# Performance work log

Measured on AMD Instinct MI355X. Metric: run time of the kernel, lower is better.

The kernel has to match this reference:

```python
import jax, jax.numpy as jnp
import numpy as np

N, IN_DIM, HID, OUT = 8192, 512, 256, 64
NEG_INF = -9e15


def setup_inputs() -> dict:
    key = jax.random.key(0)
    ks = jax.random.split(key, 7)
    X = jax.random.normal(ks[0], (N, IN_DIM), dtype=jnp.float32)
    A = jax.random.randint(ks[1], (N, N), 0, 2, dtype=jnp.int32)
    # fc1 (Linear): kaiming-uniform-ish init, exact dist irrelevant for correctness
    W1 = jax.random.normal(ks[2], (IN_DIM, HID), dtype=jnp.float32) / np.sqrt(IN_DIM)
    b1 = jnp.zeros((HID,), dtype=jnp.float32)
    # attention vector a: xavier_uniform(gain=1.414) on shape (2*HID, 1)
    lim = 1.414 * np.sqrt(6.0 / (2 * HID + 1))
    a = jax.random.uniform(ks[3], (2 * HID, 1), minval=-lim, maxval=lim, dtype=jnp.float32)
    Omega = jax.random.normal(ks[4], (HID, OUT), dtype=jnp.float32) * np.sqrt(2.0 / (HID + OUT))
    beta = jnp.zeros((OUT,), dtype=jnp.float32)
    return {"X": X, "A": A, "W1": W1, "b1": b1, "a": a, "Omega": Omega, "beta": beta}


def reference(X, A, W1, b1, a, Omega, beta):
    H1 = X @ W1 + b1                      # [N, HID]
    # score(i,j) = leakyrelu(a[:HID].H1_i + a[HID:].H1_j) -- computed via broadcast,
    # avoiding the O(N^2 * 2*HID) concat the torch code materializes.
    a1 = a[:HID, 0]                       # [HID]
    a2 = a[HID:, 0]                       # [HID]
    e = jax.nn.leaky_relu((H1 @ a1)[:, None] + (H1 @ a2)[None, :], negative_slope=0.2)  # [N, N]
    e = jnp.where(A > 0, e, NEG_INF)
    attention = jax.nn.softmax(e, axis=1)  # dropout_rate=0.0 -> identity
    H2 = attention @ H1                    # [N, HID]
    return jax.nn.sigmoid(H2 @ Omega + beta)  # [N, OUT]
```

## Files before the change

### kernel.cpp

```cpp
#include <hip/hip_runtime.h>
#include <hip/hip_bf16.h>


typedef float f32x4 __attribute__((ext_vector_type(4)));
typedef short s16x8 __attribute__((ext_vector_type(8)));

#define NN 8192
#define INDIM 512
#define HIDD 256
#define OUTD 64

static __device__ __forceinline__ short f2bf(float x) {
    __hip_bfloat16 h = __float2bfloat16(x);
    return __builtin_bit_cast(short, h);
}

static __device__ __forceinline__ void split_bf(float x, short& hi, short& lo) {
    short h = f2bf(x);
    unsigned int hb = ((unsigned int)(unsigned short)h) << 16;
    float hf = __builtin_bit_cast(float, hb);
    hi = h;
    lo = f2bf(x - hf);
}

__global__ void k_prepX(const float* __restrict__ X, short* __restrict__ XBhi) {
    int t = blockIdx.x * 256 + threadIdx.x;
    int r = t >> 9, k = t & 511;
    XBhi[(r >> 4) * 8192 + (k >> 3) * 128 + (r & 15) * 8 + (k & 7)] = f2bf(X[t]);
}

__global__ void k_prepW(const float* __restrict__ W1,
                        short* __restrict__ WBhi, short* __restrict__ WBlo) {
    int t = blockIdx.x * 256 + threadIdx.x;
    int k = t >> 8, n = t & 255;
    short h, l; split_bf(W1[t], h, l);
    int idx = (n >> 4) * 8192 + (k >> 3) * 128 + (n & 15) * 8 + (k & 7);
    WBhi[idx] = h;
    WBlo[idx] = l;
}

__global__ void __launch_bounds__(256, 2)
k_h1(const short* __restrict__ XBhi, const short* __restrict__ WBhi,
     const short* __restrict__ WBlo, const float* __restrict__ b1,
     const float* __restrict__ avec, unsigned short* __restrict__ H1TB,
     float* __restrict__ alw, float* __restrict__ bew, float* __restrict__ uvw) {
    __shared__ float s1p[4][16];
    __shared__ float s2p[4][16];
    const int tid = threadIdx.x;
    const int wn = tid >> 6, lane = tid & 63;
    const int q = lane >> 4, m16 = lane & 15;
    const int blk = blockIdx.x;

    f32x4 zero4 = {0.f, 0.f, 0.f, 0.f};
    f32x4 acc[4];
#pragma unroll
    for (int nt = 0; nt < 4; ++nt) acc[nt] = zero4;

    const short* xh = XBhi + blk * 8192 + q * 128 + m16 * 8;
    const short* wh = WBhi + wn * 4 * 8192 + q * 128 + m16 * 8;
    const short* wl = WBlo + wn * 4 * 8192 + q * 128 + m16 * 8;

    for (int c = 0; c < 16; ++c) {
        s16x8 ahi = *(const s16x8*)(xh + c * 512);
#pragma unroll
        for (int nt = 0; nt < 4; ++nt) {
            s16x8 bhi = *(const s16x8*)(wh + nt * 8192 + c * 512);
            s16x8 blo = *(const s16x8*)(wl + nt * 8192 + c * 512);
            acc[nt] = __builtin_amdgcn_mfma_f32_16x16x32_bf16(ahi, bhi, acc[nt], 0, 0, 0);
            acc[nt] = __builtin_amdgcn_mfma_f32_16x16x32_bf16(ahi, blo, acc[nt], 0, 0, 0);
        }
    }

    float p1[4] = {0.f, 0.f, 0.f, 0.f};
    float p2[4] = {0.f, 0.f, 0.f, 0.f};
#pragma unroll
    for (int nt = 0; nt < 4; ++nt) {
        const int col = wn * 64 + nt * 16 + m16;
        const float b1v = b1[col];
        const float a1v = avec[col];
        const float a2v = avec[HIDD + col];
        float v0 = acc[nt][0] + b1v;
        float v1 = acc[nt][1] + b1v;
        float v2 = acc[nt][2] + b1v;
        float v3 = acc[nt][3] + b1v;
        ushort4 us;
        us.x = (unsigned short)f2bf(v0);
        us.y = (unsigned short)f2bf(v1);
        us.z = (unsigned short)f2bf(v2);
        us.w = (unsigned short)f2bf(v3);
        const int idx = ((wn * 4 + nt) * 1024 + blk * 2 + (q >> 1)) * 128
                        + m16 * 8 + (q & 1) * 4;
        *(ushort4*)(H1TB + idx) = us;
        p1[0] += v0 * a1v; p1[1] += v1 * a1v; p1[2] += v2 * a1v; p1[3] += v3 * a1v;
        p2[0] += v0 * a2v; p2[1] += v1 * a2v; p2[2] += v2 * a2v; p2[3] += v3 * a2v;
    }
#pragma unroll
    for (int off = 1; off < 16; off <<= 1) {
#pragma unroll
        for (int r = 0; r < 4; ++r) {
            p1[r] += __shfl_xor(p1[r], off);
            p2[r] += __shfl_xor(p2[r], off);
        }
    }
    if (m16 == 0) {
#pragma unroll
        for (int r = 0; r < 4; ++r) {
            s1p[wn][q * 4 + r] = p1[r];
            s2p[wn][q * 4 + r] = p2[r];
        }
    }
    __syncthreads();
    if (tid < 16) {
        const int i = blk * 16 + tid;
        float s1 = s1p[0][tid] + s1p[1][tid] + s1p[2][tid] + s1p[3][tid];
        float s2 = s2p[0][tid] + s2p[1][tid] + s2p[2][tid] + s2p[3][tid];
        alw[i] = expf(s1);
        bew[i] = expf(0.2f * s1);
        uvw[2 * i]     = expf(s2);
        uvw[2 * i + 1] = expf(0.2f * s2);
    }
}

__global__ void __launch_bounds__(256, 4)
k_attn(const int* __restrict__ A, const unsigned short* __restrict__ H1TB,
       const float* __restrict__ alw, const float* __restrict__ bew,
       const float* __restrict__ uvw,
       float* __restrict__ H2acc, float* __restrict__ Zw) {
    const int tid = threadIdx.x;
    const int wn = tid >> 6, lane = tid & 63;
    const int q = lane >> 4, m16 = lane & 15;
    const int ks = blockIdx.x & 7;
    const int mb = blockIdx.x >> 3;
    const int row0 = mb * 32 + m16, row1 = row0 + 16;
    const float al0 = alw[row0], be0 = bew[row0];
    const float al1 = alw[row1], be1 = bew[row1];
    const int j0 = ks * 1024;

    const int* Ap0 = A + (size_t)row0 * NN + j0 + q * 8;
    const int* Ap1 = A + (size_t)row1 * NN + j0 + q * 8;
    const float* uvp = uvw + 2 * (j0 + q * 8);
    const unsigned short* Hp = H1TB + ((size_t)(wn * 4) * 1024 + ks * 128 + q) * 128 + m16 * 8;

    f32x4 zero4 = {0.f, 0.f, 0.f, 0.f};
    f32x4 acc[8];
#pragma unroll
    for (int i = 0; i < 8; ++i) acc[i] = zero4;
    float z0 = 0.f, z1 = 0.f;

    int4 a00 = *(const int4*)(Ap0);
    int4 a01 = *(const int4*)(Ap0 + 4);
    int4 a10 = *(const int4*)(Ap1);
    int4 a11 = *(const int4*)(Ap1 + 4);

    for (int t = 0; t < 32; ++t) {
        int4 n00, n01, n10, n11;
        if (t < 31) {
            n00 = *(const int4*)(Ap0 + 32);
            n01 = *(const int4*)(Ap0 + 36);
            n10 = *(const int4*)(Ap1 + 32);
            n11 = *(const int4*)(Ap1 + 36);
        }
        float4 uv0 = *(const float4*)(uvp);
        float4 uv1 = *(const float4*)(uvp + 4);
        float4 uv2 = *(const float4*)(uvp + 8);
        float4 uv3 = *(const float4*)(uvp + 12);

        float w0[8], w1[8];
        w0[0] = (a00.x > 0) ? fmaxf(al0 * uv0.x, be0 * uv0.y) : 0.f;
        w0[1] = (a00.y > 0) ? fmaxf(al0 * uv0.z, be0 * uv0.w) : 0.f;
        w0[2] = (a00.z > 0) ? fmaxf(al0 * uv1.x, be0 * uv1.y) : 0.f;
        w0[3] = (a00.w > 0) ? fmaxf(al0 * uv1.z, be0 * uv1.w) : 0.f;
        w0[4] = (a01.x > 0) ? fmaxf(al0 * uv2.x, be0 * uv2.y) : 0.f;
        w0[5] = (a01.y > 0) ? fmaxf(al0 * uv2.z, be0 * uv2.w) : 0.f;
        w0[6] = (a01.z > 0) ? fmaxf(al0 * uv3.x, be0 * uv3.y) : 0.f;
        w0[7] = (a01.w > 0) ? fmaxf(al0 * uv3.z, be0 * uv3.w) : 0.f;
        w1[0] = (a10.x > 0) ? fmaxf(al1 * uv0.x, be1 * uv0.y) : 0.f;
        w1[1] = (a10.y > 0) ? fmaxf(al1 * uv0.z, be1 * uv0.w) : 0.f;
        w1[2] = (a10.z > 0) ? fmaxf(al1 * uv1.x, be1 * uv1.y) : 0.f;
        w1[3] = (a10.w > 0) ? fmaxf(al1 * uv1.z, be1 * uv1.w) : 0.f;
        w1[4] = (a11.x > 0) ? fmaxf(al1 * uv2.x, be1 * uv2.y) : 0.f;
        w1[5] = (a11.y > 0) ? fmaxf(al1 * uv2.z, be1 * uv2.w) : 0.f;
        w1[6] = (a11.z > 0) ? fmaxf(al1 * uv3.x, be1 * uv3.y) : 0.f;
        w1[7] = (a11.w > 0) ? fmaxf(al1 * uv3.z, be1 * uv3.w) : 0.f;
        z0 += (w0[0] + w0[1] + w0[2] + w0[3]) + (w0[4] + w0[5] + w0[6] + w0[7]);
        z1 += (w1[0] + w1[1] + w1[2] + w1[3]) + (w1[4] + w1[5] + w1[6] + w1[7]);

        s16x8 af0, af1;
#pragma unroll
        for (int j = 0; j < 8; ++j) { af0[j] = f2bf(w0[j]); af1[j] = f2bf(w1[j]); }

#pragma unroll
        for (int nt = 0; nt < 4; ++nt) {
            s16x8 bf = *(const s16x8*)(Hp + (size_t)nt * 131072 + t * 512);
            acc[nt * 2 + 0] = __builtin_amdgcn_mfma_f32_16x16x32_bf16(af0, bf, acc[nt * 2 + 0], 0, 0, 0);
            acc[nt * 2 + 1] = __builtin_amdgcn_mfma_f32_16x16x32_bf16(af1, bf, acc[nt * 2 + 1], 0, 0, 0);
        }
        if (t < 31) { a00 = n00; a01 = n01; a10 = n10; a11 = n11; }
        Ap0 += 32; Ap1 += 32; uvp += 64;
    }

    z0 += __shfl_xor(z0, 16); z0 += __shfl_xor(z0, 32);
    z1 += __shfl_xor(z1, 16); z1 += __shfl_xor(z1, 32);
    if (wn == 0 && q == 0) {
        atomicAdd(&Zw[row0], z0);
        atomicAdd(&Zw[row1], z1);
    }

#pragma unroll
    for (int nt = 0; nt < 4; ++nt) {
        const int col = wn * 64 + nt * 16 + m16;
#pragma unroll
        for (int rg = 0; rg < 2; ++rg) {
            const int rowb = mb * 32 + rg * 16 + q * 4;
#pragma unroll
            for (int r = 0; r < 4; ++r)
                atomicAdd(&H2acc[(size_t)(rowb + r) * HIDD + col], acc[nt * 2 + rg][r]);
        }
    }
}

__global__ void __launch_bounds__(256)
k_out(const float* __restrict__ H2acc, const float* __restrict__ Zw,
      const float* __restrict__ Omega, const float* __restrict__ beta,
      float* __restrict__ out) {
    __shared__ float om[HIDD * OUTD];
    const int tid = threadIdx.x;
    for (int idx = tid; idx < HIDD * OUTD; idx += 256) om[idx] = Omega[idx];
    __syncthreads();
    const int wave = tid >> 6, o = tid & 63;
    const int i0 = blockIdx.x * 32 + wave * 8;
    float acc[8] = {0.f, 0.f, 0.f, 0.f, 0.f, 0.f, 0.f, 0.f};
    for (int c = 0; c < HIDD; c += 4) {
        const float o0 = om[(c + 0) * OUTD + o];
        const float o1 = om[(c + 1) * OUTD + o];
        const float o2 = om[(c + 2) * OUTD + o];
        const float o3 = om[(c + 3) * OUTD + o];
#pragma unroll
        for (int r = 0; r < 8; ++r) {
            float4 h = *(const float4*)(H2acc + (size_t)(i0 + r) * HIDD + c);
            acc[r] = fmaf(h.x, o0, fmaf(h.y, o1, fmaf(h.z, o2, fmaf(h.w, o3, acc[r]))));
        }
    }
    const float bv = beta[o];
#pragma unroll
    for (int r = 0; r < 8; ++r) {
        const float logit = acc[r] / Zw[i0 + r] + bv;
        out[(size_t)(i0 + r) * OUTD + o] = 1.0f / (1.0f + expf(-logit));
    }
}

extern "C" void kernel_launch(void* const* d_in, const int* in_sizes, int n_in,
                              void* d_out, int out_size, void* d_ws, size_t ws_size,
                              hipStream_t stream) {
    const float* X     = (const float*)d_in[0];
    const int*   A     = (const int*)d_in[1];
    const float* W1    = (const float*)d_in[2];
    const float* b1    = (const float*)d_in[3];
    const float* avec  = (const float*)d_in[4];
    const float* Omega = (const float*)d_in[5];
    const float* beta  = (const float*)d_in[6];
    float* out = (float*)d_out;

    char* ws = (char*)d_ws;
    unsigned short* H1TB = (unsigned short*)(ws + 0);
    short* XBhi  = (short*)(ws + 4194304);
    float* Zw    = (float*)(ws + 4194304);
    float* H2acc = (float*)(ws + 4227072);
    short* WBhi  = (short*)(ws + 12615680);
    short* WBlo  = (short*)(ws + 12877824);
    float* alw   = (float*)(ws + 13139968);
    float* bew   = (float*)(ws + 13172736);
    float* uvw   = (float*)(ws + 13205504);

    k_prepX<<<16384, 256, 0, stream>>>(X, XBhi);
    k_prepW<<<512, 256, 0, stream>>>(W1, WBhi, WBlo);
    k_h1<<<512, 256, 0, stream>>>(XBhi, WBhi, WBlo, b1, avec, H1TB, alw, bew, uvw);
    hipMemsetAsync(Zw, 0, 32768 + 8388608, stream);
    k_attn<<<2048, 256, 0, stream>>>(A, H1TB, alw, bew, uvw, H2acc, Zw);
    k_out<<<256, 256, 0, stream>>>(H2acc, Zw, Omega, beta, out);
}
```

Before: 566.3 us.

## Pack adjacency mask into bits before attention and retile attention waves

Adds a pre-pass that compresses the int32 adjacency matrix into a bitmask with wave ballots. A new attention kernel then reads the packed bits instead of raw ints and uses a 2x2 wave tiling over rows and hidden columns. The aim is to shrink the attention kernel's load traffic and change operand reuse, at the cost of one extra full pass over A. The old path is kept as a fallback when the workspace is too small.

```diff
diff --git a/kernel.cpp b/kernel.cpp
--- a/kernel.cpp
+++ b/kernel.cpp
@@ -13,6 +13,12 @@
 static __device__ __forceinline__ short f2bf(float x) {
     __hip_bfloat16 h = __float2bfloat16(x);
     return __builtin_bit_cast(short, h);
+}
+
+static __device__ __forceinline__ unsigned pk2bf(float a, float b) {
+    unsigned ha = (unsigned)(unsigned short)f2bf(a);
+    unsigned hb = (unsigned)(unsigned short)f2bf(b);
+    return ha | (hb << 16);
 }
 
 static __device__ __forceinline__ void split_bf(float x, short& hi, short& lo) {
@@ -37,6 +43,19 @@
     int idx = (n >> 4) * 8192 + (k >> 3) * 128 + (n & 15) * 8 + (k & 7);
     WBhi[idx] = h;
     WBlo[idx] = l;
+}
+
+__global__ void __launch_bounds__(256) k_packA(const int* __restrict__ A,
+                                               unsigned long long* __restrict__ Apk64) {
+    const int tid = threadIdx.x;
+    int f = blockIdx.x * 256 + tid;
+#pragma unroll 4
+    for (int it = 0; it < 128; ++it) {
+        int a = A[(size_t)f];
+        unsigned long long m = __ballot(a > 0);
+        if ((tid & 63) == 0) Apk64[f >> 6] = m;
+        f += 524288;
+    }
 }
 
 __global__ void __launch_bounds__(256, 2)
@@ -122,10 +141,85 @@
 }
 
 __global__ void __launch_bounds__(256, 4)
-k_attn(const int* __restrict__ A, const unsigned short* __restrict__ H1TB,
-       const float* __restrict__ alw, const float* __restrict__ bew,
-       const float* __restrict__ uvw,
-       float* __restrict__ H2acc, float* __restrict__ Zw) {
+k_attn_pk(const unsigned int* __restrict__ Apk, const unsigned short* __restrict__ H1TB,
+          const float* __restrict__ alw, const float* __restrict__ bew,
+          const float* __restrict__ uvw,
+          float* __restrict__ H2acc, float* __restrict__ Zw) {
+    const int tid = threadIdx.x;
+    const int wave = tid >> 6, lane = tid & 63;
+    const int q = lane >> 4, m16 = lane & 15;
+    const int wm = wave & 1, wn = wave >> 1;
+    const int ks = blockIdx.x & 7;
+    const int mb = blockIdx.x >> 3;
+    const int row = mb * 32 + wm * 16 + m16;
+    const float al = alw[row], be = bew[row];
+
+    const uint4* aw4 = (const uint4*)(Apk + row * 256 + ks * 32);
+    uint4 awin[8];
+#pragma unroll
+    for (int c = 0; c < 8; ++c) awin[c] = aw4[c];
+
+    const float* uvp = uvw + 2 * (ks * 1024 + q * 8);
+    const unsigned short* Hp = H1TB
+        + ((size_t)(wn * 8) * 1024 + ks * 128 + q) * 128 + m16 * 8;
+
+    f32x4 zero4 = {0.f, 0.f, 0.f, 0.f};
+    f32x4 acc[8];
+#pragma unroll
+    for (int nt = 0; nt < 8; ++nt) acc[nt] = zero4;
+    float z = 0.f;
+
+#pragma unroll
+    for (int c = 0; c < 8; ++c) {
+        unsigned int wds[4] = {awin[c].x, awin[c].y, awin[c].z, awin[c].w};
+#pragma unroll
+        for (int u = 0; u < 4; ++u) {
+            const int t = c * 4 + u;
+            const unsigned int byte = (wds[u] >> (q * 8)) & 0xFFu;
+            float4 uv0 = *(const float4*)(uvp + t * 64);
+            float4 uv1 = *(const float4*)(uvp + t * 64 + 4);
+            float4 uv2 = *(const float4*)(uvp + t * 64 + 8);
+            float4 uv3 = *(const float4*)(uvp + t * 64 + 12);
+            float w[8];
+            w[0] = (byte & 1u)   ? fmaxf(al * uv0.x, be * uv0.y) : 0.f;
+            w[1] = (byte & 2u)   ? fmaxf(al * uv0.z, be * uv0.w) : 0.f;
+            w[2] = (byte & 4u)   ? fmaxf(al * uv1.x, be * uv1.y) : 0.f;
+            w[3] = (byte & 8u)   ? fmaxf(al * uv1.z, be * uv1.w) : 0.f;
+            w[4] = (byte & 16u)  ? fmaxf(al * uv2.x, be * uv2.y) : 0.f;
+            w[5] = (byte & 32u)  ? fmaxf(al * uv2.z, be * uv2.w) : 0.f;
+            w[6] = (byte & 64u)  ? fmaxf(al * uv3.x, be * uv3.y) : 0.f;
+            w[7] = (byte & 128u) ? fmaxf(al * uv3.z, be * uv3.w) : 0.f;
+            z += (w[0] + w[1] + w[2] + w[3]) + (w[4] + w[5] + w[6] + w[7]);
+            int4 ai = {(int)pk2bf(w[0], w[1]), (int)pk2bf(w[2], w[3]),
+                       (int)pk2bf(w[4], w[5]), (int)pk2bf(w[6], w[7])};
+            s16x8 af = __builtin_bit_cast(s16x8, ai);
+#pragma unroll
+            for (int nt = 0; nt < 8; ++nt) {
+                s16x8 bf = *(const s16x8*)(Hp + (size_t)nt * 131072 + t * 512);
+                acc[nt] = __builtin_amdgcn_mfma_f32_16x16x32_bf16(af, bf, acc[nt], 0, 0, 0);
+            }
+        }
+    }
+
+    z += __shfl_xor(z, 16);
+    z += __shfl_xor(z, 32);
+    if (wn == 0 && q == 0) atomicAdd(&Zw[row], z);
+
+    const int rowb = mb * 32 + wm * 16 + q * 4;
+#pragma unroll
+    for (int nt = 0; nt < 8; ++nt) {
+        const int col = wn * 128 + nt * 16 + m16;
+#pragma unroll
+        for (int r = 0; r < 4; ++r)
+            atomicAdd(&H2acc[(size_t)(rowb + r) * HIDD + col], acc[nt][r]);
+    }
+}
+
+__global__ void __launch_bounds__(256, 4)
+k_attn_raw(const int* __restrict__ A, const unsigned short* __restrict__ H1TB,
+           const float* __restrict__ alw, const float* __restrict__ bew,
+           const float* __restrict__ uvw,
+           float* __restrict__ H2acc, float* __restrict__ Zw) {
     const int tid = threadIdx.x;
     const int wn = tid >> 6, lane = tid & 63;
     const int q = lane >> 4, m16 = lane & 15;
@@ -260,22 +354,43 @@
     const float* Omega = (const float*)d_in[5];
     const float* beta  = (const float*)d_in[6];
     float* out = (float*)d_out;
-
     char* ws = (char*)d_ws;
-    unsigned short* H1TB = (unsigned short*)(ws + 0);
-    short* XBhi  = (short*)(ws + 4194304);
-    float* Zw    = (float*)(ws + 4194304);
-    float* H2acc = (float*)(ws + 4227072);
-    short* WBhi  = (short*)(ws + 12615680);
-    short* WBlo  = (short*)(ws + 12877824);
-    float* alw   = (float*)(ws + 13139968);
-    float* bew   = (float*)(ws + 13172736);
-    float* uvw   = (float*)(ws + 13205504);
-
-    k_prepX<<<16384, 256, 0, stream>>>(X, XBhi);
-    k_prepW<<<512, 256, 0, stream>>>(W1, WBhi, WBlo);
-    k_h1<<<512, 256, 0, stream>>>(XBhi, WBhi, WBlo, b1, avec, H1TB, alw, bew, uvw);
-    hipMemsetAsync(Zw, 0, 32768 + 8388608, stream);
-    k_attn<<<2048, 256, 0, stream>>>(A, H1TB, alw, bew, uvw, H2acc, Zw);
-    k_out<<<256, 256, 0, stream>>>(H2acc, Zw, Omega, beta, out);
-}
+
+    if (ws_size >= 21659648ull) {
+        unsigned short* H1TB = (unsigned short*)(ws + 0);
+        float* Zw    = (float*)(ws + 4194304);
+        float* H2acc = (float*)(ws + 4227072);
+        short* XBhi  = (short*)(ws + 4194304);
+        unsigned int* Apk = (unsigned int*)(ws + 12615680);
+        short* WBhi  = (short*)(ws + 21004288);
+        short* WBlo  = (short*)(ws + 21266432);
+        float* alw   = (float*)(ws + 21528576);
+        float* bew   = (float*)(ws + 21561344);
+        float* uvw   = (float*)(ws + 21594112);
+
+        k_prepX<<<16384, 256, 0, stream>>>(X, XBhi);
+        k_prepW<<<512, 256, 0, stream>>>(W1, WBhi, WBlo);
+        k_h1<<<512, 256, 0, stream>>>(XBhi, WBhi, WBlo, b1, avec, H1TB, alw, bew, uvw);
+        k_packA<<<2048, 256, 0, stream>>>(A, (unsigned long long*)Apk);
+        (void)hipMemsetAsync(Zw, 0, 32768 + 8388608, stream);
+        k_attn_pk<<<2048, 256, 0, stream>>>(Apk, H1TB, alw, bew, uvw, H2acc, Zw);
+        k_out<<<256, 256, 0, stream>>>(H2acc, Zw, Omega, beta, out);
+    } else {
+        unsigned short* H1TB = (unsigned short*)(ws + 0);
+        short* XBhi  = (short*)(ws + 4194304);
+        float* Zw    = (float*)(ws + 4194304);
+        float* H2acc = (float*)(ws + 4227072);
+        short* WBhi  = (short*)(ws + 12615680);
+        short* WBlo  = (short*)(ws + 12877824);
+        float* alw   = (float*)(ws + 13139968);
+        float* bew   = (float*)(ws + 13172736);
+        float* uvw   = (float*)(ws + 13205504);
+
+        k_prepX<<<16384, 256, 0, stream>>>(X, XBhi);
+        k_prepW<<<512, 256, 0, stream>>>(W1, WBhi, WBlo);
+        k_h1<<<512, 256, 0, stream>>>(XBhi, WBhi, WBlo, b1, avec, H1TB, alw, bew, uvw);
+        (void)hipMemsetAsync(Zw, 0, 32768 + 8388608, stream);
+        k_attn_raw<<<2048, 256, 0, stream>>>(A, H1TB, alw, bew, uvw, H2acc, Zw);
+        k_out<<<256, 256, 0, stream>>>(H2acc, Zw, Omega, beta, out);
+    }
+}
```

New measurement: 849.7 us. +50.0%, slower.

## Pre-pack adjacency into bitmask and replace atomics with split partial buffers

Applied to the files above, without the earlier changes.

A new pass turns the int32 adjacency matrix into a 1-bit-per-entry mask using wave ballots, so the attention kernel reads 8 MB of mask bits instead of 256 MB of ints. The attention kernel writes per-split partial H2 and Z results to separate buffers instead of using atomicAdd, and the output kernel sums them. The number of column splits (1, 2 or 4) is chosen from the workspace size. This adds a full streaming pass over A and more workspace. With fewer splits the grid may be too small to fill the GPU.

```diff
diff --git a/kernel.cpp b/kernel.cpp
--- a/kernel.cpp
+++ b/kernel.cpp
@@ -13,6 +13,12 @@
 static __device__ __forceinline__ short f2bf(float x) {
     __hip_bfloat16 h = __float2bfloat16(x);
     return __builtin_bit_cast(short, h);
+}
+
+static __device__ __forceinline__ unsigned pk2bf(float a, float b) {
+    unsigned ha = (unsigned)(unsigned short)f2bf(a);
+    unsigned hb = (unsigned)(unsigned short)f2bf(b);
+    return ha | (hb << 16);
 }
 
 static __device__ __forceinline__ void split_bf(float x, short& hi, short& lo) {
@@ -37,6 +43,19 @@
     int idx = (n >> 4) * 8192 + (k >> 3) * 128 + (n & 15) * 8 + (k & 7);
     WBhi[idx] = h;
     WBlo[idx] = l;
+}
+
+__global__ void __launch_bounds__(256) k_packA(const int* __restrict__ A,
+                                               unsigned long long* __restrict__ Apk64) {
+    const int tid = threadIdx.x;
+    int f = blockIdx.x * 256 + tid;
+#pragma unroll 4
+    for (int it = 0; it < 128; ++it) {
+        int a = A[(size_t)f];
+        unsigned long long m = __ballot(a > 0);
+        if ((tid & 63) == 0) Apk64[f >> 6] = m;
+        f += 524288;
+    }
 }
 
 __global__ void __launch_bounds__(256, 2)
@@ -121,91 +140,102 @@
     }
 }
 
-__global__ void __launch_bounds__(256, 4)
-k_attn(const int* __restrict__ A, const unsigned short* __restrict__ H1TB,
-       const float* __restrict__ alw, const float* __restrict__ bew,
-       const float* __restrict__ uvw,
-       float* __restrict__ H2acc, float* __restrict__ Zw) {
+__global__ void __launch_bounds__(256, 3)
+k_attn_ns(const unsigned int* __restrict__ Apk, const unsigned short* __restrict__ H1TB,
+          const float* __restrict__ alw, const float* __restrict__ bew,
+          const float* __restrict__ uvw,
+          float* __restrict__ H2p, float* __restrict__ Zp, int kslog) {
     const int tid = threadIdx.x;
     const int wn = tid >> 6, lane = tid & 63;
     const int q = lane >> 4, m16 = lane & 15;
-    const int ks = blockIdx.x & 7;
-    const int mb = blockIdx.x >> 3;
+    const int ksn = 1 << kslog;
+    const int ks = blockIdx.x & (ksn - 1);
+    const int mb = blockIdx.x >> kslog;
     const int row0 = mb * 32 + m16, row1 = row0 + 16;
     const float al0 = alw[row0], be0 = bew[row0];
     const float al1 = alw[row1], be1 = bew[row1];
-    const int j0 = ks * 1024;
-
-    const int* Ap0 = A + (size_t)row0 * NN + j0 + q * 8;
-    const int* Ap1 = A + (size_t)row1 * NN + j0 + q * 8;
-    const float* uvp = uvw + 2 * (j0 + q * 8);
-    const unsigned short* Hp = H1TB + ((size_t)(wn * 4) * 1024 + ks * 128 + q) * 128 + m16 * 8;
+    const int jbase = ks << (13 - kslog);
+    const int chunks = 64 >> kslog;
+
+    const unsigned int* Ap0 = Apk + row0 * 256 + (jbase >> 5);
+    const unsigned int* Ap1 = Apk + row1 * 256 + (jbase >> 5);
+    const float* uvp = uvw + 2 * (jbase + q * 8);
+    const unsigned short* Hp = H1TB
+        + ((size_t)(wn * 4) * 1024 + (jbase >> 3) + q) * 128 + m16 * 8;
 
     f32x4 zero4 = {0.f, 0.f, 0.f, 0.f};
-    f32x4 acc[8];
-#pragma unroll
-    for (int i = 0; i < 8; ++i) acc[i] = zero4;
+    f32x4 acc[4][2];
+#pragma unroll
+    for (int nt = 0; nt < 4; ++nt) { acc[nt][0] = zero4; acc[nt][1] = zero4; }
     float z0 = 0.f, z1 = 0.f;
 
-    int4 a00 = *(const int4*)(Ap0);
-    int4 a01 = *(const int4*)(Ap0 + 4);
-    int4 a10 = *(const int4*)(Ap1);
-    int4 a11 = *(const int4*)(Ap1 + 4);
-
-    for (int t = 0; t < 32; ++t) {
-        int4 n00, n01, n10, n11;
-        if (t < 31) {
-            n00 = *(const int4*)(Ap0 + 32);
-            n01 = *(const int4*)(Ap0 + 36);
-            n10 = *(const int4*)(Ap1 + 32);
-            n11 = *(const int4*)(Ap1 + 36);
-        }
-        float4 uv0 = *(const float4*)(uvp);
-        float4 uv1 = *(const float4*)(uvp + 4);
-        float4 uv2 = *(const float4*)(uvp + 8);
-        float4 uv3 = *(const float4*)(uvp + 12);
-
-        float w0[8], w1[8];
-        w0[0] = (a00.x > 0) ? fmaxf(al0 * uv0.x, be0 * uv0.y) : 0.f;
-        w0[1] = (a00.y > 0) ? fmaxf(al0 * uv0.z, be0 * uv0.w) : 0.f;
-        w0[2] = (a00.z > 0) ? fmaxf(al0 * uv1.x, be0 * uv1.y) : 0.f;
-        w0[3] = (a00.w > 0) ? fmaxf(al0 * uv1.z, be0 * uv1.w) : 0.f;
-        w0[4] = (a01.x > 0) ? fmaxf(al0 * uv2.x, be0 * uv2.y) : 0.f;
-        w0[5] = (a01.y > 0) ? fmaxf(al0 * uv2.z, be0 * uv2.w) : 0.f;
-        w0[6] = (a01.z > 0) ? fmaxf(al0 * uv3.x, be0 * uv3.y) : 0.f;
-        w0[7] = (a01.w > 0) ? fmaxf(al0 * uv3.z, be0 * uv3.w) : 0.f;
-        w1[0] = (a10.x > 0) ? fmaxf(al1 * uv0.x, be1 * uv0.y) : 0.f;
-        w1[1] = (a10.y > 0) ? fmaxf(al1 * uv0.z, be1 * uv0.w) : 0.f;
-        w1[2] = (a10.z > 0) ? fmaxf(al1 * uv1.x, be1 * uv1.y) : 0.f;
-        w1[3] = (a10.w > 0) ? fmaxf(al1 * uv1.z, be1 * uv1.w) : 0.f;
-        w1[4] = (a11.x > 0) ? fmaxf(al1 * uv2.x, be1 * uv2.y) : 0.f;
-        w1[5] = (a11.y > 0) ? fmaxf(al1 * uv2.z, be1 * uv2.w) : 0.f;
-        w1[6] = (a11.z > 0) ? fmaxf(al1 * uv3.x, be1 * uv3.y) : 0.f;
-        w1[7] = (a11.w > 0) ? fmaxf(al1 * uv3.z, be1 * uv3.w) : 0.f;
-        z0 += (w0[0] + w0[1] + w0[2] + w0[3]) + (w0[4] + w0[5] + w0[6] + w0[7]);
-        z1 += (w1[0] + w1[1] + w1[2] + w1[3]) + (w1[4] + w1[5] + w1[6] + w1[7]);
-
-        s16x8 af0, af1;
-#pragma unroll
-        for (int j = 0; j < 8; ++j) { af0[j] = f2bf(w0[j]); af1[j] = f2bf(w1[j]); }
-
-#pragma unroll
-        for (int nt = 0; nt < 4; ++nt) {
-            s16x8 bf = *(const s16x8*)(Hp + (size_t)nt * 131072 + t * 512);
-            acc[nt * 2 + 0] = __builtin_amdgcn_mfma_f32_16x16x32_bf16(af0, bf, acc[nt * 2 + 0], 0, 0, 0);
-            acc[nt * 2 + 1] = __builtin_amdgcn_mfma_f32_16x16x32_bf16(af1, bf, acc[nt * 2 + 1], 0, 0, 0);
-        }
-        if (t < 31) { a00 = n00; a01 = n01; a10 = n10; a11 = n11; }
-        Ap0 += 32; Ap1 += 32; uvp += 64;
+    uint4 aw0 = *(const uint4*)(Ap0);
+    uint4 aw1 = *(const uint4*)(Ap1);
+
+    for (int c = 0; c < chunks; ++c) {
+        uint4 nx0, nx1;
+        if (c + 1 < chunks) {
+            nx0 = *(const uint4*)(Ap0 + 4);
+            nx1 = *(const uint4*)(Ap1 + 4);
+        }
+        unsigned wda0[4] = {aw0.x, aw0.y, aw0.z, aw0.w};
+        unsigned wda1[4] = {aw1.x, aw1.y, aw1.z, aw1.w};
+#pragma unroll
+        for (int u = 0; u < 4; ++u) {
+            const int t = c * 4 + u;
+            const unsigned b0 = (wda0[u] >> (q * 8)) & 0xFFu;
+            const unsigned b1 = (wda1[u] >> (q * 8)) & 0xFFu;
+            float4 uv0 = *(const float4*)(uvp + t * 64);
+            float4 uv1 = *(const float4*)(uvp + t * 64 + 4);
+            float4 uv2 = *(const float4*)(uvp + t * 64 + 8);
+            float4 uv3 = *(const float4*)(uvp + t * 64 + 12);
+            float w0[8], w1[8];
+            w0[0] = (b0 & 1u)   ? fmaxf(al0 * uv0.x, be0 * uv0.y) : 0.f;
+            w0[1] = (b0 & 2u)   ? fmaxf(al0 * uv0.z, be0 * uv0.w) : 0.f;
+            w0[2] = (b0 & 4u)   ? fmaxf(al0 * uv1.x, be0 * uv1.y) : 0.f;
+            w0[3] = (b0 & 8u)   ? fmaxf(al0 * uv1.z, be0 * uv1.w) : 0.f;
+            w0[4] = (b0 & 16u)  ? fmaxf(al0 * uv2.x, be0 * uv2.y) : 0.f;
+            w0[5] = (b0 & 32u)  ? fmaxf(al0 * uv2.z, be0 * uv2.w) : 0.f;
+            w0[6] = (b0 & 64u)  ? fmaxf(al0 * uv3.x, be0 * uv3.y) : 0.f;
+            w0[7] = (b0 & 128u) ? fmaxf(al0 * uv3.z, be0 * uv3.w) : 0.f;
+            w1[0] = (b1 & 1u)   ? fmaxf(al1 * uv0.x, be1 * uv0.y) : 0.f;
+            w1[1] = (b1 & 2u)   ? fmaxf(al1 * uv0.z, be1 * uv0.w) : 0.f;
+            w1[2] = (b1 & 4u)   ? fmaxf(al1 * uv1.x, be1 * uv1.y) : 0.f;
+            w1[3] = (b1 & 8u)   ? fmaxf(al1 * uv1.z, be1 * uv1.w) : 0.f;
+            w1[4] = (b1 & 16u)  ? fmaxf(al1 * uv2.x, be1 * uv2.y) : 0.f;
+            w1[5] = (b1 & 32u)  ? fmaxf(al1 * uv2.z, be1 * uv2.w) : 0.f;
+            w1[6] = (b1 & 64u)  ? fmaxf(al1 * uv3.x, be1 * uv3.y) : 0.f;
+            w1[7] = (b1 & 128u) ? fmaxf(al1 * uv3.z, be1 * uv3.w) : 0.f;
+            z0 += (w0[0] + w0[1] + w0[2] + w0[3]) + (w0[4] + w0[5] + w0[6] + w0[7]);
+            z1 += (w1[0] + w1[1] + w1[2] + w1[3]) + (w1[4] + w1[5] + w1[6] + w1[7]);
+
+            int4 ai0 = {(int)pk2bf(w0[0], w0[1]), (int)pk2bf(w0[2], w0[3]),
+                        (int)pk2bf(w0[4], w0[5]), (int)pk2bf(w0[6], w0[7])};
+            int4 ai1 = {(int)pk2bf(w1[0], w1[1]), (int)pk2bf(w1[2], w1[3]),
+                        (int)pk2bf(w1[4], w1[5]), (int)pk2bf(w1[6], w1[7])};
+            s16x8 af0 = __builtin_bit_cast(s16x8, ai0);
+            s16x8 af1 = __builtin_bit_cast(s16x8, ai1);
+#pragma unroll
+            for (int nt = 0; nt < 4; ++nt) {
+                s16x8 bf = *(const s16x8*)(Hp + (size_t)nt * 131072 + t * 512);
+                acc[nt][0] = __builtin_amdgcn_mfma_f32_16x16x32_bf16(af0, bf, acc[nt][0], 0, 0, 0);
+                acc[nt][1] = __builtin_amdgcn_mfma_f32_16x16x32_bf16(af1, bf, acc[nt][1], 0, 0, 0);
+            }
+        }
+        aw0 = nx0; aw1 = nx1;
+        Ap0 += 4; Ap1 += 4;
     }
 
     z0 += __shfl_xor(z0, 16); z0 += __shfl_xor(z0, 32);
     z1 += __shfl_xor(z1, 16); z1 += __shfl_xor(z1, 32);
     if (wn == 0 && q == 0) {
-        atomicAdd(&Zw[row0], z0);
-        atomicAdd(&Zw[row1], z1);
-    }
-
+        Zp[ks * NN + row0] = z0;
+        Zp[ks * NN + row1] = z1;
+    }
+
+    float* H2s = H2p + (size_t)ks * (NN * HIDD / 1) / (1)
+                 ;
+    H2s = H2p + (size_t)ks * 2097152;
 #pragma unroll
     for (int nt = 0; nt < 4; ++nt) {
         const int col = wn * 64 + nt * 16 + m16;
@@ -214,37 +244,42 @@
             const int rowb = mb * 32 + rg * 16 + q * 4;
 #pragma unroll
             for (int r = 0; r < 4; ++r)
-                atomicAdd(&H2acc[(size_t)(rowb + r) * HIDD + col], acc[nt * 2 + rg][r]);
+                H2s[(size_t)(rowb + r) * HIDD + col] = acc[nt][rg][r];
         }
     }
 }
 
 __global__ void __launch_bounds__(256)
-k_out(const float* __restrict__ H2acc, const float* __restrict__ Zw,
+k_out(const float* __restrict__ H2p, const float* __restrict__ Zp,
       const float* __restrict__ Omega, const float* __restrict__ beta,
-      float* __restrict__ out) {
+      float* __restrict__ out, int ksn) {
     __shared__ float om[HIDD * OUTD];
     const int tid = threadIdx.x;
     for (int idx = tid; idx < HIDD * OUTD; idx += 256) om[idx] = Omega[idx];
     __syncthreads();
     const int wave = tid >> 6, o = tid & 63;
     const int i0 = blockIdx.x * 32 + wave * 8;
-    float acc[8] = {0.f, 0.f, 0.f, 0.f, 0.f, 0.f, 0.f, 0.f};
-    for (int c = 0; c < HIDD; c += 4) {
-        const float o0 = om[(c + 0) * OUTD + o];
-        const float o1 = om[(c + 1) * OUTD + o];
-        const float o2 = om[(c + 2) * OUTD + o];
-        const float o3 = om[(c + 3) * OUTD + o];
-#pragma unroll
-        for (int r = 0; r < 8; ++r) {
-            float4 h = *(const float4*)(H2acc + (size_t)(i0 + r) * HIDD + c);
-            acc[r] = fmaf(h.x, o0, fmaf(h.y, o1, fmaf(h.z, o2, fmaf(h.w, o3, acc[r]))));
+    float accv[8] = {0.f, 0.f, 0.f, 0.f, 0.f, 0.f, 0.f, 0.f};
+    for (int s = 0; s < ksn; ++s) {
+        const float* Hs = H2p + (size_t)s * 2097152;
+        for (int c = 0; c < HIDD; c += 4) {
+            const float o0 = om[(c + 0) * OUTD + o];
+            const float o1 = om[(c + 1) * OUTD + o];
+            const float o2 = om[(c + 2) * OUTD + o];
+            const float o3 = om[(c + 3) * OUTD + o];
+#pragma unroll
+            for (int r = 0; r < 8; ++r) {
+                float4 h = *(const float4*)(Hs + (size_t)(i0 + r) * HIDD + c);
+                accv[r] = fmaf(h.x, o0, fmaf(h.y, o1, fmaf(h.z, o2, fmaf(h.w, o3, accv[r]))));
+            }
         }
     }
     const float bv = beta[o];
 #pragma unroll
     for (int r = 0; r < 8; ++r) {
-        const float logit = acc[r] / Zw[i0 + r] + bv;
+        float z = 0.f;
+        for (int s = 0; s < ksn; ++s) z += Zp[s * NN + i0 + r];
+        const float logit = accv[r] / z + bv;
         out[(size_t)(i0 + r) * OUTD + o] = 1.0f / (1.0f + expf(-logit));
     }
 }
@@ -260,22 +295,28 @@
     const float* Omega = (const float*)d_in[5];
     const float* beta  = (const float*)d_in[6];
     float* out = (float*)d_out;
-
     char* ws = (char*)d_ws;
-    unsigned short* H1TB = (unsigned short*)(ws + 0);
-    short* XBhi  = (short*)(ws + 4194304);
-    float* Zw    = (float*)(ws + 4194304);
-    float* H2acc = (float*)(ws + 4227072);
-    short* WBhi  = (short*)(ws + 12615680);
-    short* WBlo  = (short*)(ws + 12877824);
-    float* alw   = (float*)(ws + 13139968);
-    float* bew   = (float*)(ws + 13172736);
-    float* uvw   = (float*)(ws + 13205504);
+
+    int kslog = (ws_size >= 46923776ull) ? 2 : (ws_size >= 30081024ull) ? 1 : 0;
+    const int ksn = 1 << kslog;
+
+    size_t off = 0;
+    unsigned short* H1TB = (unsigned short*)(ws + off); off += 4194304;
+    unsigned int*   Apk  = (unsigned int*)(ws + off);   off += 8388608;
+    float* H2p = (float*)(ws + off);
+    short* XBhi = (short*)(ws + off);
+    off += (size_t)ksn * 8388608;
+    float* Zp  = (float*)(ws + off); off += (size_t)ksn * 32768;
+    short* WBhi = (short*)(ws + off); off += 262144;
+    short* WBlo = (short*)(ws + off); off += 262144;
+    float* alw = (float*)(ws + off); off += 32768;
+    float* bew = (float*)(ws + off); off += 32768;
+    float* uvw = (float*)(ws + off); off += 65536;
 
     k_prepX<<<16384, 256, 0, stream>>>(X, XBhi);
     k_prepW<<<512, 256, 0, stream>>>(W1, WBhi, WBlo);
     k_h1<<<512, 256, 0, stream>>>(XBhi, WBhi, WBlo, b1, avec, H1TB, alw, bew, uvw);
-    hipMemsetAsync(Zw, 0, 32768 + 8388608, stream);
-    k_attn<<<2048, 256, 0, stream>>>(A, H1TB, alw, bew, uvw, H2acc, Zw);
-    k_out<<<256, 256, 0, stream>>>(H2acc, Zw, Omega, beta, out);
-}
+    k_packA<<<2048, 256, 0, stream>>>(A, (unsigned long long*)Apk);
+    k_attn_ns<<<256 * ksn, 256, 0, stream>>>(Apk, H1TB, alw, bew, uvw, H2p, Zp, kslog);
+    k_out<<<256, 256, 0, stream>>>(H2p, Zp, Omega, beta, out, ksn);
+}
```

Result: slower. 590.5 us (+4.3%).
